# Kernel optimization log

Hardware: AMD Instinct MI355X
Metric: run time of the kernel (lower is better)

The kernel has to match this reference:

```python
import jax, jax.numpy as jnp
import numpy as np

BT, L, F, N = 8, 8192, 128, 16


def setup_inputs() -> dict:
    key = jax.random.key(0)
    ks = jax.random.split(key, 7)
    scale = 1.0 / np.sqrt(F)
    x = jax.random.normal(ks[0], (BT, L, F), dtype=jnp.float32)
    Wb = jax.random.normal(ks[1], (F, N), dtype=jnp.float32) * scale
    bb = jax.random.normal(ks[2], (N,), dtype=jnp.float32) * 0.01
    Wc = jax.random.normal(ks[3], (F, N), dtype=jnp.float32) * scale
    bc = jax.random.normal(ks[4], (N,), dtype=jnp.float32) * 0.01
    Wd = jax.random.normal(ks[5], (F, 1), dtype=jnp.float32) * scale
    bd = jax.random.normal(ks[6], (1,), dtype=jnp.float32) * 0.01
    # diagonal HiPPO-like spectrum (A is diagonal in the source: torch.diag(eigenvalues))
    A = -(jnp.arange(N, dtype=jnp.float32) + 1.0)
    return {"x": x, "Wb": Wb, "bb": bb, "Wc": Wc, "bc": bc, "Wd": Wd, "bd": bd, "A": A}


def reference(x, Wb, bb, Wc, bc, Wd, bd, A):
    # input-dependent SSM parameters (S6 / selective scan)
    B = x @ Wb + bb                      # [BT, L, N]
    C = x @ Wc + bc                      # [BT, L, N]
    delta = jax.nn.softplus(x @ Wd + bd)  # [BT, L, 1]
    # ZOH discretization with diagonal A
    dA = jnp.exp(delta * A)              # [BT, L, N]
    dB = (dA - 1.0) / A * B              # [BT, L, N]

    def step(h, inp):
        dA_t, dB_t, x_t, C_t = inp       # [BT,N],[BT,N],[BT,F],[BT,N]
        # h: [BT, F, N]; each feature channel has its own N-dim state
        h = dA_t[:, None, :] * h + dB_t[:, None, :] * x_t[:, :, None]
        y = jnp.einsum('bfn,bn->bf', h, C_t)
        return h, y

    h0 = jnp.zeros((x.shape[0], x.shape[2], A.shape[0]), dtype=x.dtype)
    xs = (jnp.swapaxes(dA, 0, 1), jnp.swapaxes(dB, 0, 1),
          jnp.swapaxes(x, 0, 1), jnp.swapaxes(C, 0, 1))
    _, ys = jax.lax.scan(step, h0, xs)   # ys: [L, BT, F]
    return jnp.swapaxes(ys, 0, 1)        # [BT, L, F]
```

## Files before the change

kernel.cpp:

```cpp
#include <hip/hip_runtime.h>


#define BTc   8
#define Lseq  8192
#define Fdim  128
#define Ndim  16
#define CH    128
#define LC    64

__global__ __launch_bounds__(256) void k_pre(
    const float* __restrict__ x,
    const float* __restrict__ Wb, const float* __restrict__ bb,
    const float* __restrict__ Wc, const float* __restrict__ bc,
    const float* __restrict__ Wd, const float* __restrict__ bd,
    const float* __restrict__ A,  float* __restrict__ G)
{
    __shared__ float Wl[33][4][36];
    const int tid = threadIdx.x;
    for (int idx = tid; idx < 33 * 128; idx += 256) {
        int j = idx >> 7, k = idx & 127;
        float v;
        if (j < 16)      v = Wb[k * 16 + j];
        else if (j < 32) v = Wc[k * 16 + (j - 16)];
        else             v = Wd[k];
        Wl[j][k >> 5][k & 31] = v;
    }
    __syncthreads();

    const int t2 = tid >> 2, ks = tid & 3;
    const size_t tokA = (size_t)blockIdx.x * 128 + t2;
    const float4* xA = reinterpret_cast<const float4*>(x + tokA * 128 + ks * 32);
    const float4* xB = reinterpret_cast<const float4*>(x + (tokA + 64) * 128 + ks * 32);

    float accA[33], accB[33];
#pragma unroll
    for (int j = 0; j < 33; ++j) { accA[j] = 0.f; accB[j] = 0.f; }

#pragma unroll 2
    for (int kk = 0; kk < 8; ++kk) {
        float4 a = xA[kk], b = xB[kk];
#pragma unroll
        for (int j = 0; j < 33; ++j) {
            float4 w = *reinterpret_cast<const float4*>(&Wl[j][ks][kk * 4]);
            accA[j] = fmaf(a.x, w.x, accA[j]);
            accA[j] = fmaf(a.y, w.y, accA[j]);
            accA[j] = fmaf(a.z, w.z, accA[j]);
            accA[j] = fmaf(a.w, w.w, accA[j]);
            accB[j] = fmaf(b.x, w.x, accB[j]);
            accB[j] = fmaf(b.y, w.y, accB[j]);
            accB[j] = fmaf(b.z, w.z, accB[j]);
            accB[j] = fmaf(b.w, w.w, accB[j]);
        }
    }

    float sel[33];
#pragma unroll
    for (int j = 0; j < 33; ++j) {
        accA[j] += __shfl_xor(accA[j], 1);
        accA[j] += __shfl_xor(accA[j], 2);
        accB[j] += __shfl_xor(accB[j], 1);
        accB[j] += __shfl_xor(accB[j], 2);
        sel[j] = (ks & 1) ? accB[j] : accA[j];
    }

    if (ks < 2) {
        const size_t tok = tokA + (size_t)(ks & 1) * 64;
        float v = sel[32] + bd[0];
        float delta = fmaxf(v, 0.f) + log1pf(expf(-fabsf(v)));
        float out[48];
#pragma unroll
        for (int n = 0; n < 16; ++n) {
            float An = A[n];
            float dA = expf(delta * An);
            float dB = (dA - 1.f) / An * (sel[n] + bb[n]);
            out[n]      = dA;
            out[16 + n] = dB;
            out[32 + n] = sel[16 + n] + bc[n];
        }
        float4* Gr = reinterpret_cast<float4*>(G + tok * 48);
#pragma unroll
        for (int p = 0; p < 12; ++p)
            Gr[p] = make_float4(out[4*p], out[4*p+1], out[4*p+2], out[4*p+3]);
    }
}

__global__ __launch_bounds__(128) void k_local(
    const float* __restrict__ x, const float* __restrict__ G,
    float* __restrict__ q, float* __restrict__ P)
{
    const int c = blockIdx.x, b = blockIdx.y;
    const int f = threadIdx.x;
    const size_t tok0 = (size_t)b * Lseq + (size_t)c * LC;
    const float4* Gp = reinterpret_cast<const float4*>(G + tok0 * 48);
    const float* xp = x + tok0 * Fdim + f;

    float h[16], pr[16];
#pragma unroll
    for (int n = 0; n < 16; ++n) { h[n] = 0.f; pr[n] = 1.f; }

#pragma unroll 2
    for (int t = 0; t < LC; ++t) {
        float4 g[8];
#pragma unroll
        for (int p = 0; p < 8; ++p) g[p] = Gp[t * 12 + p];
        float xv = xp[t * Fdim];
        const float* dA = reinterpret_cast<const float*>(&g[0]);
        const float* dB = reinterpret_cast<const float*>(&g[4]);
#pragma unroll
        for (int n = 0; n < 16; ++n) {
            h[n]  = fmaf(dA[n], h[n], dB[n] * xv);
            pr[n] *= dA[n];
        }
    }

    float4* qp = reinterpret_cast<float4*>(q + ((size_t)(b * CH + c) * 128 + f) * 16);
#pragma unroll
    for (int n4 = 0; n4 < 4; ++n4)
        qp[n4] = make_float4(h[4*n4], h[4*n4+1], h[4*n4+2], h[4*n4+3]);
    if (f == 0) {
        float4* Pp = reinterpret_cast<float4*>(P + (size_t)(b * CH + c) * 16);
#pragma unroll
        for (int n4 = 0; n4 < 4; ++n4)
            Pp[n4] = make_float4(pr[4*n4], pr[4*n4+1], pr[4*n4+2], pr[4*n4+3]);
    }
}

__global__ __launch_bounds__(256) void k_chunkscan(
    const float* __restrict__ q, const float* __restrict__ P,
    float* __restrict__ Hin)
{
    int id = blockIdx.x * 256 + threadIdx.x;
    int b  = id >> 11;
    int fn = id & 2047;
    int n  = id & 15;
    float H = 0.f;
    size_t qb = (size_t)b * CH * 2048 + fn;
    size_t pb = (size_t)b * CH * 16 + n;
    for (int cg = 0; cg < CH; cg += 16) {
        float Pr[16], qr[16];
#pragma unroll
        for (int i = 0; i < 16; ++i) {
            Pr[i] = P[pb + (size_t)(cg + i) * 16];
            qr[i] = q[qb + (size_t)(cg + i) * 2048];
        }
#pragma unroll
        for (int i = 0; i < 16; ++i) {
            Hin[qb + (size_t)(cg + i) * 2048] = H;
            H = fmaf(Pr[i], H, qr[i]);
        }
    }
}

__global__ __launch_bounds__(128) void k_final(
    const float* __restrict__ x, const float* __restrict__ G,
    const float* __restrict__ Hin, float* __restrict__ y)
{
    const int c = blockIdx.x, b = blockIdx.y;
    const int f = threadIdx.x;
    const size_t tok0 = (size_t)b * Lseq + (size_t)c * LC;
    const float4* Gp = reinterpret_cast<const float4*>(G + tok0 * 48);
    const float* xp = x + tok0 * Fdim + f;
    float*       yp = y + tok0 * Fdim + f;

    float h[16];
    const float4* hp = reinterpret_cast<const float4*>(Hin + ((size_t)(b * CH + c) * 128 + f) * 16);
#pragma unroll
    for (int n4 = 0; n4 < 4; ++n4) {
        float4 v = hp[n4];
        h[4*n4] = v.x; h[4*n4+1] = v.y; h[4*n4+2] = v.z; h[4*n4+3] = v.w;
    }

#pragma unroll 2
    for (int t = 0; t < LC; ++t) {
        float4 g[12];
#pragma unroll
        for (int p = 0; p < 12; ++p) g[p] = Gp[t * 12 + p];
        float xv = xp[t * Fdim];
        const float* dA = reinterpret_cast<const float*>(&g[0]);
        const float* dB = reinterpret_cast<const float*>(&g[4]);
        const float* Cc = reinterpret_cast<const float*>(&g[8]);
        float yacc = 0.f;
#pragma unroll
        for (int n = 0; n < 16; ++n) {
            h[n] = fmaf(dA[n], h[n], dB[n] * xv);
            yacc = fmaf(Cc[n], h[n], yacc);
        }
        yp[t * Fdim] = yacc;
    }
}

extern "C" void kernel_launch(void* const* d_in, const int* in_sizes, int n_in,
                              void* d_out, int out_size, void* d_ws, size_t ws_size,
                              hipStream_t stream) {
    const float* x  = (const float*)d_in[0];
    const float* Wb = (const float*)d_in[1];
    const float* bb = (const float*)d_in[2];
    const float* Wc = (const float*)d_in[3];
    const float* bc = (const float*)d_in[4];
    const float* Wd = (const float*)d_in[5];
    const float* bd = (const float*)d_in[6];
    const float* A  = (const float*)d_in[7];
    float* y = (float*)d_out;

    float* G   = (float*)d_ws;
    float* q   = G   + (size_t)BTc * Lseq * 48;
    float* P   = q   + (size_t)BTc * CH * Fdim * Ndim;
    float* Hin = P   + (size_t)BTc * CH * Ndim;

    k_pre<<<dim3(512), 256, 0, stream>>>(x, Wb, bb, Wc, bc, Wd, bd, A, G);
    k_local<<<dim3(CH, BTc), 128, 0, stream>>>(x, G, q, P);
    k_chunkscan<<<dim3(BTc * Fdim * Ndim / 256), 256, 0, stream>>>(q, P, Hin);
    k_final<<<dim3(CH, BTc), 128, 0, stream>>>(x, G, Hin, y);
}
```

Measured before the change: 88.55 us.

## Replace chunk decay products with delta sums and stage G rows in LDS

k_pre now reduces delta over each 64-token chunk into a per-chunk sum S. k_chunkscan rebuilds the chunk decay as exp(A*S) rather than reading a product accumulated in k_local, so k_local no longer carries the 16 running products. k_local and k_final first copy the chunk's G rows into shared memory and broadcast them from there, replacing per-thread redundant global float4 loads, and they declare a minimum of two blocks per CU. This removes redundant global traffic and some multiplies, at the cost of an extra reduction in k_pre and a __expf that may differ slightly in rounding from the direct product.

New measurement: 80.43 us. -9.2%, faster.

```diff
diff --git a/kernel.cpp b/kernel.cpp
--- a/kernel.cpp
+++ b/kernel.cpp
@@ -13,9 +13,11 @@
     const float* __restrict__ Wb, const float* __restrict__ bb,
     const float* __restrict__ Wc, const float* __restrict__ bc,
     const float* __restrict__ Wd, const float* __restrict__ bd,
-    const float* __restrict__ A,  float* __restrict__ G)
+    const float* __restrict__ A,  float* __restrict__ G,
+    float* __restrict__ S)
 {
     __shared__ float Wl[33][4][36];
+    __shared__ float Dl[2][64];
     const int tid = threadIdx.x;
     for (int idx = tid; idx < 33 * 128; idx += 256) {
         int j = idx >> 7, k = idx & 127;
@@ -67,6 +69,7 @@
         const size_t tok = tokA + (size_t)(ks & 1) * 64;
         float v = sel[32] + bd[0];
         float delta = fmaxf(v, 0.f) + log1pf(expf(-fabsf(v)));
+        Dl[ks][t2] = delta;
         float out[48];
 #pragma unroll
         for (int n = 0; n < 16; ++n) {
@@ -82,85 +85,101 @@
         for (int p = 0; p < 12; ++p)
             Gr[p] = make_float4(out[4*p], out[4*p+1], out[4*p+2], out[4*p+3]);
     }
-}
-
-__global__ __launch_bounds__(128) void k_local(
+    __syncthreads();
+
+    if (tid < 128) {
+        float val = Dl[tid >> 6][tid & 63];
+#pragma unroll
+        for (int m = 1; m < 64; m <<= 1) val += __shfl_xor(val, m);
+        if ((tid & 63) == 0) S[blockIdx.x * 2 + (tid >> 6)] = val;
+    }
+}
+
+__global__ __launch_bounds__(128, 2) void k_local(
     const float* __restrict__ x, const float* __restrict__ G,
-    float* __restrict__ q, float* __restrict__ P)
-{
+    float* __restrict__ q)
+{
+    __shared__ float Gl[LC][32];
     const int c = blockIdx.x, b = blockIdx.y;
     const int f = threadIdx.x;
     const size_t tok0 = (size_t)b * Lseq + (size_t)c * LC;
-    const float4* Gp = reinterpret_cast<const float4*>(G + tok0 * 48);
+
+    const float4* Gg = reinterpret_cast<const float4*>(G + tok0 * 48);
+    float4* Gs = reinterpret_cast<float4*>(&Gl[0][0]);
+    for (int idx = f; idx < LC * 8; idx += 128) {
+        int t = idx >> 3, p = idx & 7;
+        Gs[idx] = Gg[t * 12 + p];
+    }
+    __syncthreads();
+
+    float h[16];
+#pragma unroll
+    for (int n = 0; n < 16; ++n) h[n] = 0.f;
+
     const float* xp = x + tok0 * Fdim + f;
-
-    float h[16], pr[16];
-#pragma unroll
-    for (int n = 0; n < 16; ++n) { h[n] = 0.f; pr[n] = 1.f; }
-
 #pragma unroll 2
     for (int t = 0; t < LC; ++t) {
-        float4 g[8];
-#pragma unroll
-        for (int p = 0; p < 8; ++p) g[p] = Gp[t * 12 + p];
         float xv = xp[t * Fdim];
-        const float* dA = reinterpret_cast<const float*>(&g[0]);
-        const float* dB = reinterpret_cast<const float*>(&g[4]);
-#pragma unroll
-        for (int n = 0; n < 16; ++n) {
-            h[n]  = fmaf(dA[n], h[n], dB[n] * xv);
-            pr[n] *= dA[n];
-        }
+        const float4* gp4 = reinterpret_cast<const float4*>(&Gl[t][0]);
+        float da[16], db[16];
+#pragma unroll
+        for (int p = 0; p < 4; ++p) {
+            float4 va = gp4[p], vb = gp4[4 + p];
+            da[4*p] = va.x; da[4*p+1] = va.y; da[4*p+2] = va.z; da[4*p+3] = va.w;
+            db[4*p] = vb.x; db[4*p+1] = vb.y; db[4*p+2] = vb.z; db[4*p+3] = vb.w;
+        }
+#pragma unroll
+        for (int n = 0; n < 16; ++n)
+            h[n] = fmaf(da[n], h[n], db[n] * xv);
     }
 
     float4* qp = reinterpret_cast<float4*>(q + ((size_t)(b * CH + c) * 128 + f) * 16);
 #pragma unroll
     for (int n4 = 0; n4 < 4; ++n4)
         qp[n4] = make_float4(h[4*n4], h[4*n4+1], h[4*n4+2], h[4*n4+3]);
-    if (f == 0) {
-        float4* Pp = reinterpret_cast<float4*>(P + (size_t)(b * CH + c) * 16);
-#pragma unroll
-        for (int n4 = 0; n4 < 4; ++n4)
-            Pp[n4] = make_float4(pr[4*n4], pr[4*n4+1], pr[4*n4+2], pr[4*n4+3]);
-    }
 }
 
 __global__ __launch_bounds__(256) void k_chunkscan(
-    const float* __restrict__ q, const float* __restrict__ P,
-    float* __restrict__ Hin)
+    const float* __restrict__ q, const float* __restrict__ S,
+    const float* __restrict__ A, float* __restrict__ Hin)
 {
     int id = blockIdx.x * 256 + threadIdx.x;
     int b  = id >> 11;
     int fn = id & 2047;
     int n  = id & 15;
+    float An = A[n];
     float H = 0.f;
     size_t qb = (size_t)b * CH * 2048 + fn;
-    size_t pb = (size_t)b * CH * 16 + n;
+    const float* Sb = S + b * CH;
     for (int cg = 0; cg < CH; cg += 16) {
-        float Pr[16], qr[16];
+        float Sr[16], qr[16];
 #pragma unroll
         for (int i = 0; i < 16; ++i) {
-            Pr[i] = P[pb + (size_t)(cg + i) * 16];
+            Sr[i] = Sb[cg + i];
             qr[i] = q[qb + (size_t)(cg + i) * 2048];
         }
 #pragma unroll
         for (int i = 0; i < 16; ++i) {
             Hin[qb + (size_t)(cg + i) * 2048] = H;
-            H = fmaf(Pr[i], H, qr[i]);
-        }
-    }
-}
-
-__global__ __launch_bounds__(128) void k_final(
+            H = fmaf(__expf(An * Sr[i]), H, qr[i]);
+        }
+    }
+}
+
+__global__ __launch_bounds__(128, 2) void k_final(
     const float* __restrict__ x, const float* __restrict__ G,
     const float* __restrict__ Hin, float* __restrict__ y)
 {
+    __shared__ float Gl[LC][48];
     const int c = blockIdx.x, b = blockIdx.y;
     const int f = threadIdx.x;
     const size_t tok0 = (size_t)b * Lseq + (size_t)c * LC;
-    const float4* Gp = reinterpret_cast<const float4*>(G + tok0 * 48);
-    const float* xp = x + tok0 * Fdim + f;
-    float*       yp = y + tok0 * Fdim + f;
+
+    const float4* Gg = reinterpret_cast<const float4*>(G + tok0 * 48);
+    float4* Gs = reinterpret_cast<float4*>(&Gl[0][0]);
+    for (int idx = f; idx < LC * 12; idx += 128)
+        Gs[idx] = Gg[idx];
+    __syncthreads();
 
     float h[16];
     const float4* hp = reinterpret_cast<const float4*>(Hin + ((size_t)(b * CH + c) * 128 + f) * 16);
@@ -170,20 +189,25 @@
         h[4*n4] = v.x; h[4*n4+1] = v.y; h[4*n4+2] = v.z; h[4*n4+3] = v.w;
     }
 
+    const float* xp = x + tok0 * Fdim + f;
+    float*       yp = y + tok0 * Fdim + f;
 #pragma unroll 2
     for (int t = 0; t < LC; ++t) {
-        float4 g[12];
-#pragma unroll
-        for (int p = 0; p < 12; ++p) g[p] = Gp[t * 12 + p];
         float xv = xp[t * Fdim];
-        const float* dA = reinterpret_cast<const float*>(&g[0]);
-        const float* dB = reinterpret_cast<const float*>(&g[4]);
-        const float* Cc = reinterpret_cast<const float*>(&g[8]);
+        const float4* gp4 = reinterpret_cast<const float4*>(&Gl[t][0]);
+        float da[16], db[16], cc[16];
+#pragma unroll
+        for (int p = 0; p < 4; ++p) {
+            float4 va = gp4[p], vb = gp4[4 + p], vc = gp4[8 + p];
+            da[4*p] = va.x; da[4*p+1] = va.y; da[4*p+2] = va.z; da[4*p+3] = va.w;
+            db[4*p] = vb.x; db[4*p+1] = vb.y; db[4*p+2] = vb.z; db[4*p+3] = vb.w;
+            cc[4*p] = vc.x; cc[4*p+1] = vc.y; cc[4*p+2] = vc.z; cc[4*p+3] = vc.w;
+        }
         float yacc = 0.f;
 #pragma unroll
         for (int n = 0; n < 16; ++n) {
-            h[n] = fmaf(dA[n], h[n], dB[n] * xv);
-            yacc = fmaf(Cc[n], h[n], yacc);
+            h[n] = fmaf(da[n], h[n], db[n] * xv);
+            yacc = fmaf(cc[n], h[n], yacc);
         }
         yp[t * Fdim] = yacc;
     }
@@ -204,11 +228,11 @@
 
     float* G   = (float*)d_ws;
     float* q   = G   + (size_t)BTc * Lseq * 48;
-    float* P   = q   + (size_t)BTc * CH * Fdim * Ndim;
-    float* Hin = P   + (size_t)BTc * CH * Ndim;
-
-    k_pre<<<dim3(512), 256, 0, stream>>>(x, Wb, bb, Wc, bc, Wd, bd, A, G);
-    k_local<<<dim3(CH, BTc), 128, 0, stream>>>(x, G, q, P);
-    k_chunkscan<<<dim3(BTc * Fdim * Ndim / 256), 256, 0, stream>>>(q, P, Hin);
+    float* Hin = q   + (size_t)BTc * CH * Fdim * Ndim;
+    float* S   = Hin + (size_t)BTc * CH * Fdim * Ndim;
+
+    k_pre<<<dim3(512), 256, 0, stream>>>(x, Wb, bb, Wc, bc, Wd, bd, A, G, S);
+    k_local<<<dim3(CH, BTc), 128, 0, stream>>>(x, G, q);
+    k_chunkscan<<<dim3(BTc * Fdim * Ndim / 256), 256, 0, stream>>>(q, S, A, Hin);
     k_final<<<dim3(CH, BTc), 128, 0, stream>>>(x, G, Hin, y);
 }
```
